# Kernel tuning notes

Measured on AMD Instinct MI355X. Metric: run time of the kernel, lower is better.

The kernel has to match this reference:

```python
import jax, jax.numpy as jnp
import numpy as np

N_E = 8192
E_DIM = 256
BETA = 0.25


def setup_inputs() -> dict:
    key = jax.random.key(0)
    k_z, k_w = jax.random.split(key)
    z = jax.random.normal(k_z, (32, E_DIM, 32, 32), dtype=jnp.float32)
    # nn.Embedding weight init: uniform(-1/n_e, 1/n_e)
    W = jax.random.uniform(k_w, (N_E, E_DIM), dtype=jnp.float32,
                           minval=-1.0 / N_E, maxval=1.0 / N_E)
    return {"z": z, "W": W}


def reference(z, W):
    B, C, H, Wd = z.shape
    beta = jnp.float32(BETA)
    z_nhwc = jnp.transpose(z, (0, 2, 3, 1))          # (B,H,W,C)
    zf = z_nhwc.reshape(-1, C)                       # (N,C)
    # squared-distance matrix (N, n_e)
    d = (jnp.sum(zf * zf, axis=1, keepdims=True)
         + jnp.sum(W * W, axis=1)
         - 2.0 * jnp.matmul(zf, W.T))
    idx = jnp.argmin(d, axis=1)                      # (N,)
    # one-hot @ W == gather
    z_q = W[idx].reshape(z_nhwc.shape)               # (B,H,W,C)
    loss = (jnp.mean((jax.lax.stop_gradient(z_q) - z_nhwc) ** 2)
            + beta * jnp.mean((z_q - jax.lax.stop_gradient(z_nhwc)) ** 2))
    # straight-through estimator
    z_q = z_nhwc + jax.lax.stop_gradient(z_q - z_nhwc)
    # codebook usage perplexity
    n = idx.shape[0]
    e_mean = jnp.zeros((N_E,), jnp.float32).at[idx].add(1.0) / n
    perplexity = jnp.exp(-jnp.sum(e_mean * jnp.log(e_mean + 1e-10)))
    z_q = jnp.transpose(z_q, (0, 3, 1, 2))           # back to (B,C,H,W)
    index = idx.reshape(B, H, Wd)
    return z_q, loss, index, perplexity
```

## Files before the change

kernel.cpp:

```cpp
#include <hip/hip_runtime.h>
#include <float.h>
#include <math.h>

#define OUT_LOSS 8388608
#define OUT_IDX  8388609
#define OUT_PERP 8421377

#define WS_ZH    0ull
#define WS_ZL    16777216ull
#define WS_ZT    0ull
#define WS_WH    33554432ull
#define WS_S     37748736ull
#define WS_B     37879808ull
#define WS_MAXW  37912576ull
#define WS_IDX   37912640ull
#define WS_HIST  38043712ull
#define WS_CAND  38076480ull
#define WS_FULL  38469696ull
#define WS_FKEY  38600768ull
#define WS_CNT   38862912ull
#define WS_LOSS  38862920ull
#define WS_WL    38866944ull

typedef short v8s __attribute__((ext_vector_type(8)));
typedef float v4f __attribute__((ext_vector_type(4)));

__device__ __forceinline__ unsigned short bf16rne(float f) {
  unsigned u = __float_as_uint(f);
  return (unsigned short)((u + 0x7FFFu + ((u >> 16) & 1u)) >> 16);
}
__device__ __forceinline__ float bf16tof(unsigned short h) {
  return __uint_as_float(((unsigned)h) << 16);
}

__device__ __forceinline__ void gl_lds16(const void* g, void* l) {
  __builtin_amdgcn_global_load_lds(
      (const __attribute__((address_space(1))) unsigned int*)g,
      (__attribute__((address_space(3))) unsigned int*)l, 16, 0, 0);
}

__global__ void k_zero(int* __restrict__ hist, unsigned long long* __restrict__ fkey,
                       int* __restrict__ cnt, double* __restrict__ loss,
                       unsigned* __restrict__ maxw) {
  const int i = blockIdx.x * 256 + threadIdx.x;
  if (i < 8192) hist[i] = 0;
  else if (i < 40960) fkey[i - 8192] = ~0ull;
  else if (i == 40960) cnt[0] = 0;
  else if (i == 40961) cnt[1] = 0;
  else if (i == 40962) *loss = 0.0;
  else if (i == 40963) *maxw = 0u;
}

__global__ __launch_bounds__(256) void k_split(const float* __restrict__ W,
                                               unsigned short* __restrict__ Wh,
                                               unsigned short* __restrict__ Wl) {
  const int u = blockIdx.x * 256 + threadIdx.x;
  const int kc = u >> 15, grp = (u >> 6) & 511, q = (u >> 4) & 3, col = u & 15;
  const int j = grp * 16 + col, k0 = kc * 32 + q * 8;
  const float4 w0 = *(const float4*)(W + (size_t)j * 256 + k0);
  const float4 w1 = *(const float4*)(W + (size_t)j * 256 + k0 + 4);
  const float wv[8] = {w0.x, w0.y, w0.z, w0.w, w1.x, w1.y, w1.z, w1.w};
  unsigned short h[8] __attribute__((aligned(16)));
  unsigned short l[8] __attribute__((aligned(16)));
#pragma unroll
  for (int i = 0; i < 8; ++i) {
    h[i] = bf16rne(wv[i]);
    l[i] = bf16rne(__fsub_rn(wv[i], bf16tof(h[i])));
  }
  *(uint4*)(Wh + (size_t)u * 8) = *(const uint4*)h;
  *(uint4*)(Wl + (size_t)u * 8) = *(const uint4*)l;
}

__global__ __launch_bounds__(256) void k_splitz(const float* __restrict__ z,
    unsigned short* __restrict__ Zh, unsigned short* __restrict__ Zl) {
  const int gt = blockIdx.x * 256 + threadIdx.x;
  const int kc = gt >> 15;
  const int n  = gt & 32767;
  const int b = n >> 10, p = n & 1023;
  const float* zp = z + (size_t)b * 262144 + (size_t)(kc * 32) * 1024 + p;
  unsigned short hh[32] __attribute__((aligned(16)));
  unsigned short ll[32] __attribute__((aligned(16)));
#pragma unroll
  for (int i = 0; i < 32; ++i) {
    const float v = zp[(size_t)i * 1024];
    const unsigned short h = bf16rne(v);
    hh[i] = h;
    ll[i] = bf16rne(__fsub_rn(v, bf16tof(h)));
  }
  const size_t o = (size_t)kc * 1048576 + (size_t)(n >> 4) * 512 + (size_t)(n & 15) * 8;
#pragma unroll
  for (int q = 0; q < 4; ++q) *(uint4*)(Zh + o + q * 128) = *(const uint4*)(hh + q * 8);
#pragma unroll
  for (int q = 0; q < 4; ++q) *(uint4*)(Zl + o + q * 128) = *(const uint4*)(ll + q * 8);
}

__global__ __launch_bounds__(256) void k_zt(const float* __restrict__ z,
                                            float* __restrict__ zT) {
  const int gt = blockIdx.x * 256 + threadIdx.x;
  const int kc = gt >> 15;
  const int n  = gt & 32767;
  const int b = n >> 10, p = n & 1023;
  const float* zp = z + (size_t)b * 262144 + (size_t)(kc * 32) * 1024 + p;
  float v[32] __attribute__((aligned(16)));
#pragma unroll
  for (int i = 0; i < 32; ++i) v[i] = zp[(size_t)i * 1024];
  float* dst = zT + (size_t)n * 256 + kc * 32;
#pragma unroll
  for (int j = 0; j < 8; ++j) *(float4*)(dst + j * 4) = *(const float4*)(v + j * 4);
}

__device__ __forceinline__ float np_sumsq256(const float* __restrict__ base,
                                             const int stride) {
  float h[2];
#pragma unroll
  for (int half = 0; half < 2; ++half) {
    const float* a = base + (size_t)(half * 128) * stride;
    float r[8];
#pragma unroll
    for (int k = 0; k < 8; ++k) { const float v = a[(size_t)k * stride]; r[k] = __fmul_rn(v, v); }
    for (int i = 8; i < 128; i += 8) {
#pragma unroll
      for (int k = 0; k < 8; ++k) {
        const float v = a[(size_t)(i + k) * stride];
        r[k] = __fadd_rn(r[k], __fmul_rn(v, v));
      }
    }
    h[half] = __fadd_rn(
        __fadd_rn(__fadd_rn(r[0], r[1]), __fadd_rn(r[2], r[3])),
        __fadd_rn(__fadd_rn(r[4], r[5]), __fadd_rn(r[6], r[7])));
  }
  return __fadd_rn(h[0], h[1]);
}

__global__ __launch_bounds__(256) void k_sz(const float* __restrict__ z,
                                            float* __restrict__ S) {
  const int n = blockIdx.x * 256 + threadIdx.x;
  S[n] = np_sumsq256(z + (size_t)(n >> 10) * 262144 + (n & 1023), 1024);
}

__global__ __launch_bounds__(256) void k_wsq(const float* __restrict__ W,
                                             float* __restrict__ B,
                                             unsigned* __restrict__ maxw) {
  const int j = blockIdx.x * 256 + threadIdx.x;
  const float b = np_sumsq256(W + (size_t)j * 256, 1);
  B[j] = b;
  atomicMax(maxw, __float_as_uint(b));
}

__device__ __forceinline__ void merge5(float& a1, int& ai1, float& a2, int& ai2,
                                       float& a3, float b1, int bi1, float b2,
                                       int bi2, float b3) {
  const bool t1 = (b1 < a1) || (b1 == a1 && bi1 < ai1);
  const float w2v = t1 ? b2 : a2; const int w2i = t1 ? bi2 : ai2;
  const float w3v = t1 ? b3 : a3;
  const float l1v = t1 ? a1 : b1; const int l1i = t1 ? ai1 : bi1;
  const float l2v = t1 ? a2 : b2;
  const float n1v = t1 ? b1 : a1; const int n1i = t1 ? bi1 : ai1;
  const bool t2 = (w2v < l1v) || (w2v == l1v && w2i < l1i);
  a1 = n1v; ai1 = n1i;
  a2 = t2 ? w2v : l1v; ai2 = t2 ? w2i : l1i;
  a3 = t2 ? fminf(w3v, l1v) : fminf(w2v, l2v);
}

#define AH_OFF   0
#define AL_OFF   32768
#define B0_OFF   65536
#define B1_OFF   98304
#define SC_OFF   65536
#define SMEM_SZ  131072
__global__ __launch_bounds__(512, 1) void k_main(
    const unsigned short* __restrict__ Zh, const unsigned short* __restrict__ Zl,
    const unsigned short* __restrict__ Wh, const unsigned short* __restrict__ Wl,
    const float* __restrict__ S, const float* __restrict__ B,
    const unsigned* __restrict__ maxw, int* __restrict__ idxb,
    int* __restrict__ cand, int* __restrict__ full, int* __restrict__ cnt) {
  extern __shared__ __align__(16) char smem[];
  const int t = threadIdx.x;
  const int w = t >> 6, lane = t & 63, col = lane & 15, q = lane >> 4;
  const int phalf = w >> 2, strip = w & 3;
  const int n0 = blockIdx.x << 6;

  float spx[8];
#pragma unroll
  for (int s = 0; s < 8; ++s)
    spx[s] = S[n0 + phalf * 32 + (s >> 2) * 16 + q * 4 + (s & 3)];

  {
    const size_t ab = (size_t)w * 1048576 + (size_t)(n0 >> 4) * 512 + (size_t)lane * 8;
    char* dh = smem + AH_OFF + w * 4096;
    char* dl = smem + AL_OFF + w * 4096;
#pragma unroll
    for (int i = 0; i < 4; ++i) gl_lds16(Zh + ab + (size_t)i * 512, dh + i * 1024);
#pragma unroll
    for (int i = 0; i < 4; ++i) gl_lds16(Zl + ab + (size_t)i * 512, dl + i * 1024);
  }
  {
    const size_t bb = (size_t)(w * 4) * 512 + (size_t)lane * 8;
#pragma unroll
    for (int i = 0; i < 4; ++i)
      gl_lds16(Wh + bb + (size_t)i * 512, smem + B0_OFF + (w * 4 + i) * 1024);
  }
  v8s bl[8];
  {
    const unsigned short* p = Wl + (size_t)(strip * 8) * 512 + (size_t)lane * 8;
#pragma unroll
    for (int nt = 0; nt < 8; ++nt) bl[nt] = *(const v8s*)(p + nt * 512);
  }
  __syncthreads();

  float m1[8], m2[8], m3[8]; int i1[8], i2[8];
#pragma unroll
  for (int s = 0; s < 8; ++s) {
    m1[s] = FLT_MAX; m2[s] = FLT_MAX; m3[s] = FLT_MAX;
    i1[s] = 0x7fffffff; i2[s] = 0x7fffffff;
  }

  v4f acc[2][8];
#pragma unroll
  for (int pt = 0; pt < 2; ++pt)
#pragma unroll
    for (int nt = 0; nt < 8; ++nt) acc[pt][nt] = (v4f){0.f, 0.f, 0.f, 0.f};

  for (int ct = 0; ct < 16; ++ct) {
#pragma unroll
    for (int kc = 0; kc < 8; ++kc) {
      const int it = ct * 8 + kc;
      if (it < 127) {
        const int nc = it + 1;
        const size_t cb = (size_t)(nc & 7) * 262144 + (size_t)(nc >> 3) * 16384
                        + (size_t)(w * 4) * 512 + (size_t)lane * 8;
        char* nh = smem + ((nc & 1) ? B1_OFF : B0_OFF) + (w * 4) * 1024;
#pragma unroll
        for (int i = 0; i < 4; ++i)
          gl_lds16(Wh + cb + (size_t)i * 512, nh + i * 1024);
      }
      const char* bhb = smem + ((it & 1) ? B1_OFF : B0_OFF);
      const int nc2 = (it + 1) & 127;
      const unsigned short* blsrc = Wl + (size_t)(nc2 & 7) * 262144
                                  + (size_t)(nc2 >> 3) * 16384
                                  + (size_t)(strip * 8) * 512 + (size_t)lane * 8;
      v8s ah[2], al[2];
#pragma unroll
      for (int pt = 0; pt < 2; ++pt) {
        const int g = phalf * 2 + pt;
        ah[pt] = *(const v8s*)(smem + AH_OFF + kc * 4096 + g * 1024 + lane * 16);
        al[pt] = *(const v8s*)(smem + AL_OFF + kc * 4096 + g * 1024 + lane * 16);
      }
#pragma unroll
      for (int nt = 0; nt < 8; ++nt) {
        const v8s bh = *(const v8s*)(bhb + (strip * 8 + nt) * 1024 + lane * 16);
        const v8s blv = bl[nt];
#pragma unroll
        for (int pt = 0; pt < 2; ++pt) {
          acc[pt][nt] = __builtin_amdgcn_mfma_f32_16x16x32_bf16(ah[pt], bh, acc[pt][nt], 0, 0, 0);
          acc[pt][nt] = __builtin_amdgcn_mfma_f32_16x16x32_bf16(al[pt], bh, acc[pt][nt], 0, 0, 0);
          acc[pt][nt] = __builtin_amdgcn_mfma_f32_16x16x32_bf16(ah[pt], blv, acc[pt][nt], 0, 0, 0);
        }
        bl[nt] = *(const v8s*)(blsrc + nt * 512);
      }
      __syncthreads();
      if (kc == 7) {
#pragma unroll
        for (int nt = 0; nt < 8; ++nt) {
          const int code = ct * 512 + strip * 128 + nt * 16 + col;
          const float bb = B[code];
#pragma unroll
          for (int pt = 0; pt < 2; ++pt) {
            const v4f a = acc[pt][nt];
#pragma unroll
            for (int r = 0; r < 4; ++r) {
              const int s = pt * 4 + r;
              const float d = __fsub_rn(__fadd_rn(spx[s], bb), __fmul_rn(2.f, a[r]));
              const bool c1 = (d < m1[s]);
              const bool c2 = (d < m2[s]);
              const bool c3 = (d < m3[s]);
              m3[s] = c2 ? m2[s] : (c3 ? d : m3[s]);
              m2[s] = c1 ? m1[s] : (c2 ? d : m2[s]);
              i2[s] = c1 ? i1[s] : (c2 ? code : i2[s]);
              m1[s] = c1 ? d : m1[s];
              i1[s] = c1 ? code : i1[s];
            }
          }
#pragma unroll
          for (int pt = 0; pt < 2; ++pt) acc[pt][nt] = (v4f){0.f, 0.f, 0.f, 0.f};
        }
      }
    }
  }

#pragma unroll
  for (int s = 0; s < 8; ++s) {
    for (int msk = 1; msk < 16; msk <<= 1) {
      const float b1 = __shfl_xor(m1[s], msk, 16);
      const int  bi1 = __shfl_xor(i1[s], msk, 16);
      const float b2 = __shfl_xor(m2[s], msk, 16);
      const int  bi2 = __shfl_xor(i2[s], msk, 16);
      const float b3 = __shfl_xor(m3[s], msk, 16);
      merge5(m1[s], i1[s], m2[s], i2[s], m3[s], b1, bi1, b2, bi2, b3);
    }
  }
  __syncthreads();
  float* sc = (float*)(smem + SC_OFF);
  if (col == 0) {
#pragma unroll
    for (int s = 0; s < 8; ++s) {
      const int px = phalf * 32 + (s >> 2) * 16 + q * 4 + (s & 3);
      const int base = (px * 4 + strip) * 5;
      sc[base]     = m1[s];
      sc[base + 1] = __int_as_float(i1[s]);
      sc[base + 2] = m2[s];
      sc[base + 3] = __int_as_float(i2[s]);
      sc[base + 4] = m3[s];
    }
  }
  __syncthreads();
  if (t < 64) {
    const int base0 = t * 20;
    float A1 = sc[base0], A2 = sc[base0 + 2], A3 = sc[base0 + 4];
    int AI1 = __float_as_int(sc[base0 + 1]), AI2 = __float_as_int(sc[base0 + 3]);
    for (int st = 1; st < 4; ++st) {
      const int base = base0 + st * 5;
      merge5(A1, AI1, A2, AI2, A3, sc[base], __float_as_int(sc[base + 1]),
             sc[base + 2], __float_as_int(sc[base + 3]), sc[base + 4]);
    }
    const int n = n0 + t;
    idxb[n] = AI1;
    const float nw = sqrtf(S[n]) * sqrtf(__uint_as_float(*maxw));
    const float win = 2.0f * (1.52587890625e-05f * nw + 1e-6f)
                    + 2.0f * ldexpf(1.0f, ilogbf(fmaxf(A1, 1e-30f)) - 23);
    if (A2 <= A1 + win) {
      if (A3 <= A1 + win) {
        const int p = atomicAdd(&cnt[1], 1);
        full[p] = n;
      } else {
        const int p = atomicAdd(&cnt[0], 1);
        cand[3 * p] = n; cand[3 * p + 1] = AI1; cand[3 * p + 2] = AI2;
      }
    }
  }
}

__global__ __launch_bounds__(256) void k_cand(const float* __restrict__ zT,
    const float* __restrict__ W, const float* __restrict__ S,
    const float* __restrict__ B, const int* __restrict__ cand,
    const int* __restrict__ cnt, int* __restrict__ idxb) {
  const int e = blockIdx.x * 256 + threadIdx.x;
  if (e >= cnt[0]) return;
  const int n = cand[3 * e], ca = cand[3 * e + 1], cb = cand[3 * e + 2];
  const float* zp = zT + (size_t)n * 256;
  const float* wa = W + (size_t)ca * 256;
  const float* wb = W + (size_t)cb * 256;
  float a1 = 0.f, a2 = 0.f;
  for (int c = 0; c < 256; ++c) {
    const float zv = zp[c];
    a1 = __builtin_fmaf(zv, wa[c], a1);
    a2 = __builtin_fmaf(zv, wb[c], a2);
  }
  const float d1 = __fsub_rn(__fadd_rn(S[n], B[ca]), __fmul_rn(2.f, a1));
  const float d2 = __fsub_rn(__fadd_rn(S[n], B[cb]), __fmul_rn(2.f, a2));
  idxb[n] = (d1 < d2) ? ca : ((d2 < d1) ? cb : min(ca, cb));
}

__global__ __launch_bounds__(256) void k_full(const float* __restrict__ zT,
    const float* __restrict__ W, const float* __restrict__ S,
    const float* __restrict__ B, const int* __restrict__ full,
    const int* __restrict__ cnt, unsigned long long* __restrict__ fkey) {
  extern __shared__ __align__(16) char fsm[];
  float* zsf = (float*)fsm;
  float* wt  = (float*)(fsm + 32768);
  float* mv  = (float*)(fsm + 32768 + 32896);
  int*   mi  = (int*)(fsm + 32768 + 32896 + 4224);
  const int t = threadIdx.x;
  const int pg = t & 7, cg = t >> 3;
  const int fN = min(cnt[1], 32768);
  const int units = ((fN + 31) >> 5) << 5;
  for (int e = blockIdx.x; e < units; e += 2048) {
    const int g = e >> 5, tt = e & 31;
    const int c0 = tt << 8;
    __syncthreads();
    {
      const int px = t >> 3, c8 = t & 7;
      const int f = (g << 5) + px;
      const int n = (f < fN) ? full[f] : full[0];
      const float4* src = (const float4*)(zT + (size_t)n * 256 + c8 * 32);
      const int colq = (((px >> 2) ^ c8) << 2) + (px & 3);
#pragma unroll
      for (int j = 0; j < 8; ++j) {
        const float4 v = src[j];
        const int c = c8 * 32 + j * 4;
        zsf[(c    ) * 32 + colq] = v.x;
        zsf[(c + 1) * 32 + colq] = v.y;
        zsf[(c + 2) * 32 + colq] = v.z;
        zsf[(c + 3) * 32 + colq] = v.w;
      }
    }
    float s4[4];
#pragma unroll
    for (int i = 0; i < 4; ++i) {
      const int f = (g << 5) + (pg << 2) + i;
      s4[i] = (f < fN) ? S[full[f]] : 0.f;
    }
    float bm[4]; int bj[4];
#pragma unroll
    for (int i = 0; i < 4; ++i) { bm[i] = FLT_MAX; bj[i] = 0x7fffffff; }
    float acc[4][8];
#pragma unroll
    for (int i = 0; i < 4; ++i)
#pragma unroll
      for (int u = 0; u < 8; ++u) acc[i][u] = 0.f;
    for (int kc = 0; kc < 8; ++kc) {
      const int kb = kc << 5;
      __syncthreads();
#pragma unroll
      for (int p = 0; p < 8; ++p) {
        const int jl = (t >> 3) + (p << 5);
        const float4 wv4 =
            *(const float4*)&W[(size_t)(c0 + jl) * 256 + kb + ((t & 7) << 2)];
        const int k0 = (t & 7) << 2;
        wt[(k0    ) * 257 + jl] = wv4.x;
        wt[(k0 + 1) * 257 + jl] = wv4.y;
        wt[(k0 + 2) * 257 + jl] = wv4.z;
        wt[(k0 + 3) * 257 + jl] = wv4.w;
      }
      __syncthreads();
      const int zq = ((pg ^ kc) & 7) << 2;
      for (int k = 0; k < 32; ++k) {
        const float4 z4 = *(const float4*)&zsf[(kb + k) * 32 + zq];
        const float4 wA = *(const float4*)&wt[k * 257 + (cg << 3)];
        const float4 wB = *(const float4*)&wt[k * 257 + (cg << 3) + 4];
        const float zv[4] = {z4.x, z4.y, z4.z, z4.w};
        const float wv[8] = {wA.x, wA.y, wA.z, wA.w, wB.x, wB.y, wB.z, wB.w};
#pragma unroll
        for (int i = 0; i < 4; ++i)
#pragma unroll
          for (int u = 0; u < 8; ++u)
            acc[i][u] = __builtin_fmaf(zv[i], wv[u], acc[i][u]);
      }
    }
#pragma unroll
    for (int u = 0; u < 8; ++u) {
      const int code = c0 + (cg << 3) + u;
      const float bb = B[code];
#pragma unroll
      for (int i = 0; i < 4; ++i) {
        const float d = __fsub_rn(__fadd_rn(s4[i], bb), __fmul_rn(2.f, acc[i][u]));
        if (d < bm[i]) { bm[i] = d; bj[i] = code; }
      }
    }
    __syncthreads();
#pragma unroll
    for (int i = 0; i < 4; ++i) {
      const int px = (pg << 2) + i;
      mv[px * 33 + cg] = bm[i];
      mi[px * 33 + cg] = bj[i];
    }
    __syncthreads();
    if (t < 32) {
      float m = mv[t * 33]; int j = mi[t * 33];
      for (int c = 1; c < 32; ++c) {
        const float v = mv[t * 33 + c]; const int vi = mi[t * 33 + c];
        if (v < m || (v == m && vi < j)) { m = v; j = vi; }
      }
      const int f = (g << 5) + t;
      if (f < fN) {
        const unsigned long long key =
            (((unsigned long long)__float_as_uint(m)) << 13) | (unsigned)j;
        atomicMin(&fkey[f], key);
      }
    }
  }
}

__global__ __launch_bounds__(256) void k_fullfin(const int* __restrict__ full,
    const int* __restrict__ cnt, const unsigned long long* __restrict__ fkey,
    int* __restrict__ idxb) {
  const int f = blockIdx.x * 256 + threadIdx.x;
  if (f < cnt[1]) idxb[full[f]] = (int)(fkey[f] & 8191ull);
}

__global__ __launch_bounds__(256) void k_zq(const float* __restrict__ z,
    const float* __restrict__ W, const int* __restrict__ idxb,
    float* __restrict__ out, double* __restrict__ loss, int* __restrict__ hist) {
  __shared__ float red[256];
  const int t = threadIdx.x;
  const int tx = t & 63, ty = t >> 6;
  const int n0 = blockIdx.x << 6;
  const int n = n0 + tx;
  const int b = n >> 10;
  const int p = n & 1023;
  const int myidx = idxb[n];
  const float* wrow = W + (size_t)myidx * 256;
  float lsum = 0.f;
#pragma unroll 4
  for (int cc = 0; cc < 64; ++cc) {
    const int c = ty * 64 + cc;
    const float qv = wrow[c];
    const size_t off = (size_t)b * 262144 + (size_t)c * 1024 + p;
    const float zv = z[off];
    const float d = __fsub_rn(qv, zv);
    lsum = __builtin_fmaf(d, d, lsum);
    out[off] = __fadd_rn(zv, d);
  }
  red[t] = lsum;
  __syncthreads();
  for (int o = 128; o > 0; o >>= 1) {
    if (t < o) red[t] += red[t + o];
    __syncthreads();
  }
  if (t == 0) atomicAdd(loss, (double)red[0]);
  if (ty == 0) atomicAdd(&hist[myidx], 1);
  if (ty == 1) out[OUT_IDX + n] = (float)myidx;
}

__global__ void k_final(const int* __restrict__ hist,
                        const double* __restrict__ loss,
                        float* __restrict__ out) {
  __shared__ double sh[256];
  const int t = threadIdx.x;
  double s = 0.0;
  for (int j = t; j < 8192; j += 256) {
    const double e = (double)hist[j] / 32768.0;
    s += e * log(e + 1e-10);
  }
  sh[t] = s;
  __syncthreads();
  for (int off = 128; off > 0; off >>= 1) {
    if (t < off) sh[t] += sh[t + off];
    __syncthreads();
  }
  if (t == 0) {
    out[OUT_PERP] = (float)exp(-sh[0]);
    out[OUT_LOSS] = (float)(1.25 * (*loss) / 8388608.0);
  }
}

extern "C" void kernel_launch(void* const* d_in, const int* in_sizes, int n_in,
                              void* d_out, int out_size, void* d_ws, size_t ws_size,
                              hipStream_t stream) {
  const float* z = (const float*)d_in[0];
  const float* W = (const float*)d_in[1];
  float* out = (float*)d_out;
  char* ws = (char*)d_ws;
  unsigned short* Zh = (unsigned short*)(ws + WS_ZH);
  unsigned short* Zl = (unsigned short*)(ws + WS_ZL);
  unsigned short* Wh = (unsigned short*)(ws + WS_WH);
  unsigned short* Wl = (unsigned short*)(ws + WS_WL);
  float*  zT   = (float*)(ws + WS_ZT);
  float*  S    = (float*)(ws + WS_S);
  float*  B    = (float*)(ws + WS_B);
  unsigned* maxw = (unsigned*)(ws + WS_MAXW);
  int*    idxb = (int*)(ws + WS_IDX);
  int*    hist = (int*)(ws + WS_HIST);
  int*    cand = (int*)(ws + WS_CAND);
  int*    full = (int*)(ws + WS_FULL);
  unsigned long long* fkey = (unsigned long long*)(ws + WS_FKEY);
  int*    cnt  = (int*)(ws + WS_CNT);
  double* loss = (double*)(ws + WS_LOSS);

  hipLaunchKernelGGL(k_zero,    dim3(161),  dim3(256), 0, stream, hist, fkey, cnt, loss, maxw);
  hipLaunchKernelGGL(k_split,   dim3(1024), dim3(256), 0, stream, W, Wh, Wl);
  hipLaunchKernelGGL(k_splitz,  dim3(1024), dim3(256), 0, stream, z, Zh, Zl);
  hipLaunchKernelGGL(k_sz,      dim3(128),  dim3(256), 0, stream, z, S);
  hipLaunchKernelGGL(k_wsq,     dim3(32),   dim3(256), 0, stream, W, B, maxw);
  hipLaunchKernelGGL(k_main,    dim3(512),  dim3(512), SMEM_SZ, stream,
                     Zh, Zl, Wh, Wl, S, B, maxw, idxb, cand, full, cnt);
  hipLaunchKernelGGL(k_zt,      dim3(1024), dim3(256), 0, stream, z, zT);
  hipLaunchKernelGGL(k_cand,    dim3(128),  dim3(256), 0, stream, zT, W, S, B, cand, cnt, idxb);
  hipLaunchKernelGGL(k_full,    dim3(2048), dim3(256), 74112, stream, zT, W, S, B, full, cnt, fkey);
  hipLaunchKernelGGL(k_fullfin, dim3(128),  dim3(256), 0, stream, full, cnt, fkey, idxb);
  hipLaunchKernelGGL(k_zq,      dim3(512),  dim3(256), 0, stream, z, W, idxb, out, loss, hist);
  hipLaunchKernelGGL(k_final,   dim3(1),    dim3(256), 0, stream, hist, loss, out);
}
```

Before: 795.7 us.

## Load codebook fragments straight from global into registers, drop LDS double buffer

The codebook high part no longer goes through a double-buffered LDS stage. Each wave now loads both its high and low bf16 codebook fragments directly from global memory into registers, prefetching one fragment ahead, and the per-iteration block barrier is removed. With LDS halved to 64 KB, launch bounds now allow two 512-thread blocks per CU. The MFMA calls are reordered so the two row tiles alternate, which spreads out accumulator dependencies. In exchange, every wave fetches codebook data from global/L2 separately with only one step of lookahead, so latency may be exposed and cache traffic goes up.

```diff
diff --git a/kernel.cpp b/kernel.cpp
--- a/kernel.cpp
+++ b/kernel.cpp
@@ -164,11 +164,9 @@
 
 #define AH_OFF   0
 #define AL_OFF   32768
-#define B0_OFF   65536
-#define B1_OFF   98304
-#define SC_OFF   65536
-#define SMEM_SZ  131072
-__global__ __launch_bounds__(512, 1) void k_main(
+#define SC_OFF   0
+#define SMEM_SZ  65536
+__global__ __launch_bounds__(512, 2) void k_main(
     const unsigned short* __restrict__ Zh, const unsigned short* __restrict__ Zl,
     const unsigned short* __restrict__ Wh, const unsigned short* __restrict__ Wl,
     const float* __restrict__ S, const float* __restrict__ B,
@@ -194,18 +192,10 @@
 #pragma unroll
     for (int i = 0; i < 4; ++i) gl_lds16(Zl + ab + (size_t)i * 512, dl + i * 1024);
   }
-  {
-    const size_t bb = (size_t)(w * 4) * 512 + (size_t)lane * 8;
-#pragma unroll
-    for (int i = 0; i < 4; ++i)
-      gl_lds16(Wh + bb + (size_t)i * 512, smem + B0_OFF + (w * 4 + i) * 1024);
-  }
-  v8s bl[8];
-  {
-    const unsigned short* p = Wl + (size_t)(strip * 8) * 512 + (size_t)lane * 8;
-#pragma unroll
-    for (int nt = 0; nt < 8; ++nt) bl[nt] = *(const v8s*)(p + nt * 512);
-  }
+  const unsigned short* pWh = Wh + (size_t)(strip * 8) * 512 + (size_t)lane * 8;
+  const unsigned short* pWl = Wl + (size_t)(strip * 8) * 512 + (size_t)lane * 8;
+  v8s bhc = *(const v8s*)pWh;
+  v8s blc = *(const v8s*)pWl;
   __syncthreads();
 
   float m1[8], m2[8], m3[8]; int i1[8], i2[8];
@@ -224,41 +214,25 @@
   for (int ct = 0; ct < 16; ++ct) {
 #pragma unroll
     for (int kc = 0; kc < 8; ++kc) {
-      const int it = ct * 8 + kc;
-      if (it < 127) {
-        const int nc = it + 1;
-        const size_t cb = (size_t)(nc & 7) * 262144 + (size_t)(nc >> 3) * 16384
-                        + (size_t)(w * 4) * 512 + (size_t)lane * 8;
-        char* nh = smem + ((nc & 1) ? B1_OFF : B0_OFF) + (w * 4) * 1024;
-#pragma unroll
-        for (int i = 0; i < 4; ++i)
-          gl_lds16(Wh + cb + (size_t)i * 512, nh + i * 1024);
-      }
-      const char* bhb = smem + ((it & 1) ? B1_OFF : B0_OFF);
-      const int nc2 = (it + 1) & 127;
-      const unsigned short* blsrc = Wl + (size_t)(nc2 & 7) * 262144
-                                  + (size_t)(nc2 >> 3) * 16384
-                                  + (size_t)(strip * 8) * 512 + (size_t)lane * 8;
-      v8s ah[2], al[2];
-#pragma unroll
-      for (int pt = 0; pt < 2; ++pt) {
-        const int g = phalf * 2 + pt;
-        ah[pt] = *(const v8s*)(smem + AH_OFF + kc * 4096 + g * 1024 + lane * 16);
-        al[pt] = *(const v8s*)(smem + AL_OFF + kc * 4096 + g * 1024 + lane * 16);
-      }
+      const v8s ah0 = *(const v8s*)(smem + AH_OFF + kc * 4096 + (phalf * 2 + 0) * 1024 + lane * 16);
+      const v8s ah1 = *(const v8s*)(smem + AH_OFF + kc * 4096 + (phalf * 2 + 1) * 1024 + lane * 16);
+      const v8s al0 = *(const v8s*)(smem + AL_OFF + kc * 4096 + (phalf * 2 + 0) * 1024 + lane * 16);
+      const v8s al1 = *(const v8s*)(smem + AL_OFF + kc * 4096 + (phalf * 2 + 1) * 1024 + lane * 16);
 #pragma unroll
       for (int nt = 0; nt < 8; ++nt) {
-        const v8s bh = *(const v8s*)(bhb + (strip * 8 + nt) * 1024 + lane * 16);
-        const v8s blv = bl[nt];
-#pragma unroll
-        for (int pt = 0; pt < 2; ++pt) {
-          acc[pt][nt] = __builtin_amdgcn_mfma_f32_16x16x32_bf16(ah[pt], bh, acc[pt][nt], 0, 0, 0);
-          acc[pt][nt] = __builtin_amdgcn_mfma_f32_16x16x32_bf16(al[pt], bh, acc[pt][nt], 0, 0, 0);
-          acc[pt][nt] = __builtin_amdgcn_mfma_f32_16x16x32_bf16(ah[pt], blv, acc[pt][nt], 0, 0, 0);
-        }
-        bl[nt] = *(const v8s*)(blsrc + nt * 512);
-      }
-      __syncthreads();
+        const int f = ((ct * 8 + kc) * 8 + nt + 1) & 1023;
+        const size_t noff = (size_t)((f >> 3) & 7) * 262144
+                          + (size_t)(f >> 6) * 16384 + (size_t)(f & 7) * 512;
+        const v8s bhn = *(const v8s*)(pWh + noff);
+        const v8s bln = *(const v8s*)(pWl + noff);
+        acc[0][nt] = __builtin_amdgcn_mfma_f32_16x16x32_bf16(ah0, bhc, acc[0][nt], 0, 0, 0);
+        acc[1][nt] = __builtin_amdgcn_mfma_f32_16x16x32_bf16(ah1, bhc, acc[1][nt], 0, 0, 0);
+        acc[0][nt] = __builtin_amdgcn_mfma_f32_16x16x32_bf16(al0, bhc, acc[0][nt], 0, 0, 0);
+        acc[1][nt] = __builtin_amdgcn_mfma_f32_16x16x32_bf16(al1, bhc, acc[1][nt], 0, 0, 0);
+        acc[0][nt] = __builtin_amdgcn_mfma_f32_16x16x32_bf16(ah0, blc, acc[0][nt], 0, 0, 0);
+        acc[1][nt] = __builtin_amdgcn_mfma_f32_16x16x32_bf16(ah1, blc, acc[1][nt], 0, 0, 0);
+        bhc = bhn; blc = bln;
+      }
       if (kc == 7) {
 #pragma unroll
         for (int nt = 0; nt < 8; ++nt) {
```

Result: slower. 1.513 ms (+90.1%).
